# Kernel optimization log

Measured on AMD Instinct MI355X. Metric: run time of the kernel, lower is better.

Reference implementation:

```python
import jax, jax.numpy as jnp
import numpy as np

# ---- static config (matches init_kwargs) ----
B, S, D = 2, 4096, 1024          # batch, seq_len, dim_input
L, ST = 512, 64                  # segment_len, state_len
H = 8                            # num_heads
DK0, DV0, DK1, DV1 = 64, 64, 64, 64  # per-head key/value dims for 2 memory levels
DH = 4096                        # dim_hidden (MLP)
T = 2 * ST + L                   # tokens per segment block: [state, segment, state]


def setup_inputs() -> dict:
    key = jax.random.key(0)
    ks = jax.random.split(key, 18)
    f32 = jnp.float32
    def w(k, shape, fan_in):
        return (jax.random.normal(k, shape, dtype=f32) / np.float32(np.sqrt(fan_in)))
    return {
        "x": jax.random.normal(ks[0], (B, S, D), dtype=f32),
        "state_init": 0.02 * jax.random.normal(ks[1], (ST, D), dtype=f32),
        # level-0 projections: dim_input -> per-head (key/value)
        "Wq0": w(ks[2], (D, H, DK0), D),
        "Wk0": w(ks[3], (D, H, DK0), D),
        "Wv0": w(ks[4], (D, H, DV0), D),
        # level-1 projections: level-0 value dim -> per-head (key/value)
        "Wq1": w(ks[5], (H, DV0, DK1), DV0),
        "Wk1": w(ks[6], (H, DV0, DK1), DV0),
        "Wv1": w(ks[7], (H, DV0, DV1), DV0),
        # output projection back to dim_input
        "Wo": w(ks[8], (H, DV1, D), H * DV1),
        "bo": jnp.zeros((D,), f32),
        "g_attn": jnp.ones((D,), f32),
        "b_attn": jnp.zeros((D,), f32),
        "W1": w(ks[9], (D, DH), D),
        "b1": jnp.zeros((DH,), f32),
        "W2": w(ks[10], (DH, D), DH),
        "b2": jnp.zeros((D,), f32),
        "g_mlp": jnp.ones((D,), f32),
        "b_mlp": jnp.zeros((D,), f32),
    }


def _layernorm(x, g, b, eps=1e-5):
    mu = jnp.mean(x, axis=-1, keepdims=True)
    var = jnp.mean(jnp.square(x - mu), axis=-1, keepdims=True)
    return (x - mu) * jax.lax.rsqrt(var + eps) * g + b


def _rope(x, pos):
    # x: (B, H, T, dk); rotary embedding with base 10000
    dk = x.shape[-1]
    inv_freq = jnp.power(jnp.float32(10000.0), -jnp.arange(0, dk, 2, dtype=jnp.float32) / dk)
    ang = pos[:, None] * inv_freq[None, :]              # (T, dk/2)
    cos, sin = jnp.cos(ang), jnp.sin(ang)
    x1, x2 = x[..., 0::2], x[..., 1::2]
    r1 = x1 * cos - x2 * sin
    r2 = x1 * sin + x2 * cos
    return jnp.stack([r1, r2], axis=-1).reshape(x.shape)


def _attend(q, k, v, mask):
    # q,k: (B,H,T,dk); v: (B,H,T,dv); causal mask (T,T)
    scale = jnp.float32(1.0 / np.sqrt(q.shape[-1]))
    scores = jnp.einsum('bhqc,bhkc->bhqk', q, k) * scale
    scores = jnp.where(mask, scores, jnp.float32(-1e30))
    p = jax.nn.softmax(scores, axis=-1)
    return jnp.einsum('bhqk,bhkv->bhqv', p, v)


def _remmtas(x, state_init, Wq0, Wk0, Wv0, Wq1, Wk1, Wv1, Wo, bo):
    b, s, d = x.shape
    n_seg = s // L
    xs = x.reshape(b, n_seg, L, d).transpose(1, 0, 2, 3)   # (n_seg, B, L, D)
    mask = jnp.tril(jnp.ones((T, T), dtype=bool))
    pos = jnp.arange(T, dtype=jnp.float32)
    state0 = jnp.broadcast_to(state_init, (b, ST, d))

    def step(state, seg):
        toks = jnp.concatenate([state, seg, state], axis=1)      # (B, T, D)
        # memory level 0
        q0 = _rope(jnp.einsum('btd,dhk->bhtk', toks, Wq0), pos)
        k0 = _rope(jnp.einsum('btd,dhk->bhtk', toks, Wk0), pos)
        v0 = jnp.einsum('btd,dhv->bhtv', toks, Wv0)
        o0 = _attend(q0, k0, v0, mask)                           # (B,H,T,DV0)
        # memory level 1 (consumes level-0 values, per-head)
        q1 = _rope(jnp.einsum('bhtv,hvk->bhtk', o0, Wq1), pos)
        k1 = _rope(jnp.einsum('bhtv,hvk->bhtk', o0, Wk1), pos)
        v1 = jnp.einsum('bhtv,hvw->bhtw', o0, Wv1)
        o1 = _attend(q1, k1, v1, mask)                           # (B,H,T,DV1)
        out = jnp.einsum('bhtv,hvd->btd', o1, Wo) + bo           # (B,T,D)
        new_state = out[:, ST + L:]                              # trailing state tokens
        return new_state, out[:, ST:ST + L]                      # segment output

    _, outs = jax.lax.scan(step, state0, xs)                     # (n_seg, B, L, D)
    return outs.transpose(1, 0, 2, 3).reshape(b, s, d)


def reference(x, state_init, Wq0, Wk0, Wv0, Wq1, Wk1, Wv1, Wo, bo,
              g_attn, b_attn, W1, b1, W2, b2, g_mlp, b_mlp):
    a = _remmtas(x, state_init, Wq0, Wk0, Wv0, Wq1, Wk1, Wv1, Wo, bo)
    h = _layernorm(a + x, g_attn, b_attn)
    m = jax.nn.gelu(h @ W1 + b1, approximate=False) @ W2 + b2
    # note: second residual adds the ORIGINAL x, per the source code
    return _layernorm(m + x, g_mlp, b_mlp)
```

## Files before the change

kernel.cpp:

```cpp
#include <hip/hip_runtime.h>
#include <hip/hip_bf16.h>

typedef __hip_bfloat16 bf16;
typedef short bf16x8 __attribute__((ext_vector_type(8)));
typedef float f32x4 __attribute__((ext_vector_type(4)));

#define CB 2
#define CS 4096
#define CD 1024
#define CL 512
#define CST 64
#define CH 8
#define CT 640
#define CDH 4096
#define NSEG 8
#define MCH 2048
#define LP 80

__device__ __forceinline__ float tof(float x) { return x; }
__device__ __forceinline__ float tof(bf16 x) { return __bfloat162float(x); }
__device__ __forceinline__ void storev(float* p, float v) { *p = v; }
__device__ __forceinline__ void storev(bf16* p, float v) { *p = __float2bfloat16(v); }

__device__ __forceinline__ float ldin(const void* p, size_t i, int f32w) {
    if (f32w) return ((const float*)p)[i];
    return __bfloat162float(((const bf16*)p)[i]);
}

__global__ void sniff_kernel(const void* x, int* flag) {
    if (threadIdx.x == 0 && blockIdx.x == 0) {
        const bf16* hb = (const bf16*)x;
        int plaus = 0;
        for (int i = 0; i < 256; ++i) {
            float v = __bfloat162float(hb[2 * i]);
            float a = fabsf(v);
            if (v == 0.f || (a > 1e-4f && a < 100.f)) ++plaus;
        }
        flag[0] = (plaus < 128) ? 1 : 0;
    }
}

__global__ __launch_bounds__(256) void transpose_kernel(
    const void* __restrict__ in, bf16* __restrict__ out, int R, int C,
    const int* __restrict__ flag)
{
    const int f32w = flag[0];
    __shared__ short t[64][72];
    int tid = threadIdx.x;
    int c0 = blockIdx.x * 64, r0 = blockIdx.y * 64;
    int cc = tid & 63, rr = tid >> 6;
#pragma unroll
    for (int i = 0; i < 16; ++i) {
        bf16 v = __float2bfloat16(ldin(in, (size_t)(r0 + rr + i * 4) * C + c0 + cc, f32w));
        t[rr + i * 4][cc] = *(short*)&v;
    }
    __syncthreads();
#pragma unroll
    for (int i = 0; i < 16; ++i)
        ((short*)out)[(size_t)(c0 + rr + i * 4) * R + r0 + cc] = t[cc][rr + i * 4];
}

__global__ __launch_bounds__(256) void transposeH_kernel(
    const void* __restrict__ Wq1, const void* __restrict__ Wk1, const void* __restrict__ Wv1,
    bf16* __restrict__ oq, bf16* __restrict__ ok, bf16* __restrict__ ov,
    const int* __restrict__ flag)
{
    const int f32w = flag[0];
    int which = blockIdx.x >> 3, hh = blockIdx.x & 7;
    const void* in = (which == 0) ? Wq1 : (which == 1) ? Wk1 : Wv1;
    bf16* out = (which == 0) ? oq : (which == 1) ? ok : ov;
    __shared__ short t[64][72];
    int tid = threadIdx.x;
    int cc = tid & 63, rr = tid >> 6;
    size_t base = (size_t)hh * 4096;
#pragma unroll
    for (int i = 0; i < 16; ++i) {
        bf16 v = __float2bfloat16(ldin(in, base + (size_t)(rr + i * 4) * 64 + cc, f32w));
        t[rr + i * 4][cc] = *(short*)&v;
    }
    __syncthreads();
#pragma unroll
    for (int i = 0; i < 16; ++i)
        ((short*)out)[base + (size_t)(rr + i * 4) * 64 + cc] = t[cc][rr + i * 4];
}

template <typename TC, int ACT, int OUTM, int KSPLIT>
__global__ __launch_bounds__(256) void mfma_lds(
    const bf16* __restrict__ A,
    const bf16* __restrict__ Bt0, const bf16* __restrict__ Bt1, const bf16* __restrict__ Bt2,
    TC* __restrict__ C0, TC* __restrict__ C1, TC* __restrict__ C2,
    const void* __restrict__ bias, int M, int N, int K, int seg,
    const int* __restrict__ flag)
{
    const int f32w = flag[0];
    const bf16* Bt = (blockIdx.z == 0) ? Bt0 : (blockIdx.z == 1 ? Bt1 : Bt2);
    TC* C = (blockIdx.z == 0) ? C0 : (blockIdx.z == 1 ? C1 : C2);
    const int kz = (KSPLIT > 1) ? (int)blockIdx.z : 0;
    const int kbeg = (KSPLIT > 1) ? kz * (K / KSPLIT) : 0;
    const int kend = (KSPLIT > 1) ? kbeg + K / KSPLIT : K;

    __shared__ __align__(16) short As[128 * 64];
    __shared__ __align__(16) short Bs[128 * 64];

    const int tid = threadIdx.x;
    const int lane = tid & 63;
    const int w = tid >> 6;
    const int wm = w >> 1, wn = w & 1;
    const int bm = blockIdx.x * 128, bn = blockIdx.y * 128;

    f32x4 acc[4][4];
#pragma unroll
    for (int i = 0; i < 4; ++i)
#pragma unroll
        for (int j = 0; j < 4; ++j) acc[i][j] = (f32x4){0.f, 0.f, 0.f, 0.f};

    bf16x8 rA[4], rB[4];
#pragma unroll
    for (int i = 0; i < 4; ++i) {
        int c = i * 256 + tid;
        int row = c >> 3, kc = c & 7;
        rA[i] = *(const bf16x8*)(A + (size_t)(bm + row) * K + kbeg + kc * 8);
        rB[i] = *(const bf16x8*)(Bt + (size_t)(bn + row) * K + kbeg + kc * 8);
    }

    for (int k0 = kbeg; k0 < kend; k0 += 64) {
        __syncthreads();
#pragma unroll
        for (int i = 0; i < 4; ++i) {
            *(bf16x8*)&As[(size_t)(i * 256 + tid) * 8] = rA[i];
            *(bf16x8*)&Bs[(size_t)(i * 256 + tid) * 8] = rB[i];
        }
        if (k0 + 64 < kend) {
            int kn = k0 + 64;
#pragma unroll
            for (int i = 0; i < 4; ++i) {
                int c = i * 256 + tid;
                int row = c >> 3, kc = c & 7;
                rA[i] = *(const bf16x8*)(A + (size_t)(bm + row) * K + kn + kc * 8);
                rB[i] = *(const bf16x8*)(Bt + (size_t)(bn + row) * K + kn + kc * 8);
            }
        }
        __syncthreads();

#pragma unroll
        for (int kh = 0; kh < 2; ++kh) {
            bf16x8 av[4], bv[4];
#pragma unroll
            for (int mi = 0; mi < 4; ++mi) {
                int r = wm * 64 + mi * 16 + (lane & 15);
                int cl = kh * 4 + (lane >> 4);
                av[mi] = *(const bf16x8*)&As[r * 64 + cl * 8];
            }
#pragma unroll
            for (int nj = 0; nj < 4; ++nj) {
                int r = wn * 64 + nj * 16 + (lane & 15);
                int cl = kh * 4 + (lane >> 4);
                bv[nj] = *(const bf16x8*)&Bs[r * 64 + cl * 8];
            }
#pragma unroll
            for (int mi = 0; mi < 4; ++mi)
#pragma unroll
                for (int nj = 0; nj < 4; ++nj)
                    acc[mi][nj] = __builtin_amdgcn_mfma_f32_16x16x32_bf16(
                        av[mi], bv[nj], acc[mi][nj], 0, 0, 0);
        }
    }

#pragma unroll
    for (int mi = 0; mi < 4; ++mi) {
#pragma unroll
        for (int nj = 0; nj < 4; ++nj) {
            int c = bn + wn * 64 + nj * 16 + (lane & 15);
            float bia = (bias && kz == 0) ? ldin(bias, c, f32w) : 0.f;
#pragma unroll
            for (int r = 0; r < 4; ++r) {
                int row = bm + wm * 64 + mi * 16 + (lane >> 4) * 4 + r;
                float v = acc[mi][nj][r] + bia;
                if (ACT == 1) v = 0.5f * v * (1.0f + erff(v * 0.70710678118654752f));
                if (KSPLIT > 1) {
                    atomicAdd((float*)C + (size_t)row * N + c, v);
                } else if (OUTM == 0) {
                    storev(C + (size_t)row * N + c, v);
                } else {
                    int bb2 = row / CT, t = row % CT;
                    if (t >= CST) {
                        if (t < CST + CL)
                            storev(C0 + ((size_t)bb2 * CS + (size_t)seg * CL + (t - CST)) * CD + c, v);
                        else
                            storev(C1 + ((size_t)bb2 * CST + (t - CST - CL)) * CD + c, v);
                    }
                }
            }
        }
    }
}

__global__ __launch_bounds__(256) void ropeV_kernel(
    bf16* __restrict__ q, bf16* __restrict__ k,
    const bf16* __restrict__ v, bf16* __restrict__ vt)
{
    int t0 = blockIdx.x * 64, hh = blockIdx.y, b = blockIdx.z;
    int tid = threadIdx.x;
    __shared__ short lt[64][72];
    int c = tid & 63;
    int r0 = tid >> 6;
    int ip = c >> 1;
    float inv = powf(10000.f, -(float)(2 * ip) / 64.f);
#pragma unroll
    for (int i = 0; i < 16; ++i) {
        int r = r0 + i * 4;
        int t = t0 + r;
        size_t idx = ((size_t)b * CT + t) * 512 + hh * 64 + c;
        float qv = tof(q[idx]);
        float kv = tof(k[idx]);
        float ang = (float)t * inv;
        float sn, cs;
        sincosf(ang, &sn, &cs);
        float qp = __shfl_xor(qv, 1);
        float kp = __shfl_xor(kv, 1);
        float rq, rk;
        if (c & 1) { rq = qp * sn + qv * cs; rk = kp * sn + kv * cs; }
        else       { rq = qv * cs - qp * sn; rk = kv * cs - kp * sn; }
        q[idx] = __float2bfloat16(rq);
        k[idx] = __float2bfloat16(rk);
        lt[r][c] = ((const short*)v)[idx];
    }
    __syncthreads();
#pragma unroll
    for (int i = 0; i < 16; ++i) {
        int c2 = r0 + i * 4;
        int r2 = c;
        ((short*)vt)[((size_t)(b * CH + hh) * 64 + c2) * CT + t0 + r2] = lt[r2][c2];
    }
}

template <int FUSE>
__global__ __launch_bounds__(256) void attn_mfma(
    const bf16* __restrict__ q, const bf16* __restrict__ k, const bf16* __restrict__ vt,
    bf16* __restrict__ o,
    int qsb, int qsh, int qst,
    int ksb, int ksh, int kst,
    int ob, int oh, int ot,
    const bf16* __restrict__ Wq1t, const bf16* __restrict__ Wk1t, const bf16* __restrict__ Wv1t,
    bf16* __restrict__ q1o, bf16* __restrict__ k1o, bf16* __restrict__ v1to)
{
    const int tid = threadIdx.x;
    const int lane = tid & 63;
    const int wrow = tid >> 6;
    const int hh = blockIdx.y, b = blockIdx.z;
    const int qbase = ((int)gridDim.x - 1 - (int)blockIdx.x) * 64;

    __shared__ __align__(16) short Qs[64 * LP];
    __shared__ __align__(16) short Ks[64 * LP];
    __shared__ __align__(16) short Vs[64 * LP];
    __shared__ __align__(16) short Ps[64 * LP];

    const size_t qb0 = (size_t)b * qsb + (size_t)hh * qsh;
    const size_t kb0 = (size_t)b * ksb + (size_t)hh * ksh;
    const size_t vtb = (size_t)(b * CH + hh) * 64 * CT;

    int srow[2], skc[2], soff[2];
#pragma unroll
    for (int i = 0; i < 2; ++i) {
        int c = i * 256 + tid;
        srow[i] = c >> 3;
        skc[i] = c & 7;
        soff[i] = srow[i] * LP + skc[i] * 8;
    }

    bf16x8 rQ[2], rK[2], rV[2];
#pragma unroll
    for (int i = 0; i < 2; ++i) {
        rQ[i] = *(const bf16x8*)(q + qb0 + (size_t)(qbase + srow[i]) * qst + skc[i] * 8);
        rK[i] = *(const bf16x8*)(k + kb0 + (size_t)srow[i] * kst + skc[i] * 8);
        rV[i] = *(const bf16x8*)(vt + vtb + (size_t)srow[i] * CT + skc[i] * 8);
    }

    float mrow[4], lrow[4];
    f32x4 oacc[4];
#pragma unroll
    for (int r = 0; r < 4; ++r) { mrow[r] = -1e30f; lrow[r] = 0.f; }
#pragma unroll
    for (int nd = 0; nd < 4; ++nd) oacc[nd] = (f32x4){0.f, 0.f, 0.f, 0.f};

    const int ntiles = qbase / 64 + 1;
    for (int ti = 0; ti < ntiles; ++ti) {
        __syncthreads();
        if (ti == 0) {
#pragma unroll
            for (int i = 0; i < 2; ++i) *(bf16x8*)&Qs[soff[i]] = rQ[i];
        }
#pragma unroll
        for (int i = 0; i < 2; ++i) {
            *(bf16x8*)&Ks[soff[i]] = rK[i];
            *(bf16x8*)&Vs[soff[i]] = rV[i];
        }
        if (ti + 1 < ntiles) {
            int j1 = (ti + 1) * 64;
#pragma unroll
            for (int i = 0; i < 2; ++i) {
                rK[i] = *(const bf16x8*)(k + kb0 + (size_t)(j1 + srow[i]) * kst + skc[i] * 8);
                rV[i] = *(const bf16x8*)(vt + vtb + (size_t)srow[i] * CT + j1 + skc[i] * 8);
            }
        }
        __syncthreads();

        f32x4 sacc[4];
#pragma unroll
        for (int nj = 0; nj < 4; ++nj) sacc[nj] = (f32x4){0.f, 0.f, 0.f, 0.f};
#pragma unroll
        for (int kh = 0; kh < 2; ++kh) {
            int cl = kh * 4 + (lane >> 4);
            bf16x8 av = *(const bf16x8*)&Qs[(wrow * 16 + (lane & 15)) * LP + cl * 8];
#pragma unroll
            for (int nj = 0; nj < 4; ++nj) {
                bf16x8 bv = *(const bf16x8*)&Ks[(nj * 16 + (lane & 15)) * LP + cl * 8];
                sacc[nj] = __builtin_amdgcn_mfma_f32_16x16x32_bf16(av, bv, sacc[nj], 0, 0, 0);
            }
        }

        const bool diag = (ti == ntiles - 1);
        float pm[4] = {-1e30f, -1e30f, -1e30f, -1e30f};
#pragma unroll
        for (int nj = 0; nj < 4; ++nj) {
            int col_l = nj * 16 + (lane & 15);
#pragma unroll
            for (int r = 0; r < 4; ++r) {
                int row_l = wrow * 16 + ((lane >> 4) << 2) + r;
                float s = (diag && col_l > row_l) ? -1e30f : sacc[nj][r] * 0.125f;
                sacc[nj][r] = s;
                pm[r] = fmaxf(pm[r], s);
            }
        }
#pragma unroll
        for (int msk = 1; msk < 16; msk <<= 1)
#pragma unroll
            for (int r = 0; r < 4; ++r) pm[r] = fmaxf(pm[r], __shfl_xor(pm[r], msk));

        float corr[4], rs[4] = {0.f, 0.f, 0.f, 0.f};
#pragma unroll
        for (int r = 0; r < 4; ++r) {
            float mn = fmaxf(mrow[r], pm[r]);
            corr[r] = __expf(mrow[r] - mn);
            mrow[r] = mn;
        }
#pragma unroll
        for (int nj = 0; nj < 4; ++nj)
#pragma unroll
            for (int r = 0; r < 4; ++r) {
                float p = __expf(sacc[nj][r] - mrow[r]);
                sacc[nj][r] = p;
                rs[r] += p;
            }
#pragma unroll
        for (int msk = 1; msk < 16; msk <<= 1)
#pragma unroll
            for (int r = 0; r < 4; ++r) rs[r] += __shfl_xor(rs[r], msk);
#pragma unroll
        for (int r = 0; r < 4; ++r) lrow[r] = lrow[r] * corr[r] + rs[r];
#pragma unroll
        for (int nd = 0; nd < 4; ++nd)
#pragma unroll
            for (int r = 0; r < 4; ++r) oacc[nd][r] *= corr[r];

#pragma unroll
        for (int nj = 0; nj < 4; ++nj)
#pragma unroll
            for (int r = 0; r < 4; ++r) {
                bf16 pb = __float2bfloat16(sacc[nj][r]);
                Ps[(wrow * 16 + ((lane >> 4) << 2) + r) * LP + nj * 16 + (lane & 15)] =
                    *(short*)&pb;
            }

#pragma unroll
        for (int kh = 0; kh < 2; ++kh) {
            int cl = kh * 4 + (lane >> 4);
            bf16x8 pa = *(const bf16x8*)&Ps[(wrow * 16 + (lane & 15)) * LP + cl * 8];
#pragma unroll
            for (int nd = 0; nd < 4; ++nd) {
                bf16x8 bv = *(const bf16x8*)&Vs[(nd * 16 + (lane & 15)) * LP + cl * 8];
                oacc[nd] = __builtin_amdgcn_mfma_f32_16x16x32_bf16(pa, bv, oacc[nd], 0, 0, 0);
            }
        }
    }

    if (FUSE == 0) {
#pragma unroll
        for (int nd = 0; nd < 4; ++nd) {
#pragma unroll
            for (int r = 0; r < 4; ++r) {
                int row_g = qbase + wrow * 16 + ((lane >> 4) << 2) + r;
                int col = nd * 16 + (lane & 15);
                storev(&o[(size_t)b * ob + (size_t)hh * oh + (size_t)row_g * ot + col],
                       oacc[nd][r] / lrow[r]);
            }
        }
    } else {
#pragma unroll
        for (int nd = 0; nd < 4; ++nd)
#pragma unroll
            for (int r = 0; r < 4; ++r) {
                int row_l = wrow * 16 + ((lane >> 4) << 2) + r;
                bf16 ob16 = __float2bfloat16(oacc[nd][r] / lrow[r]);
                Qs[row_l * LP + nd * 16 + (lane & 15)] = *(short*)&ob16;
            }
        __syncthreads();

        const size_t whb = (size_t)hh * 4096;
        f32x4 qa[4], ka[4], va[4];
#pragma unroll
        for (int nj = 0; nj < 4; ++nj) {
            qa[nj] = (f32x4){0.f, 0.f, 0.f, 0.f};
            ka[nj] = (f32x4){0.f, 0.f, 0.f, 0.f};
            va[nj] = (f32x4){0.f, 0.f, 0.f, 0.f};
        }
#pragma unroll
        for (int kh = 0; kh < 2; ++kh) {
            int cl = kh * 4 + (lane >> 4);
            bf16x8 av = *(const bf16x8*)&Qs[(wrow * 16 + (lane & 15)) * LP + cl * 8];
#pragma unroll
            for (int nj = 0; nj < 4; ++nj) {
                int rowb = nj * 16 + (lane & 15);
                bf16x8 bq = *(const bf16x8*)(Wq1t + whb + (size_t)rowb * 64 + cl * 8);
                bf16x8 bk = *(const bf16x8*)(Wk1t + whb + (size_t)rowb * 64 + cl * 8);
                bf16x8 bw = *(const bf16x8*)(Wv1t + whb + (size_t)rowb * 64 + cl * 8);
                qa[nj] = __builtin_amdgcn_mfma_f32_16x16x32_bf16(av, bq, qa[nj], 0, 0, 0);
                ka[nj] = __builtin_amdgcn_mfma_f32_16x16x32_bf16(av, bk, ka[nj], 0, 0, 0);
                va[nj] = __builtin_amdgcn_mfma_f32_16x16x32_bf16(av, bw, va[nj], 0, 0, 0);
            }
        }
        const size_t bh = (size_t)(b * CH + hh);
#pragma unroll
        for (int nj = 0; nj < 4; ++nj) {
            int col = nj * 16 + (lane & 15);
            int ip = col >> 1;
            float inv = powf(10000.f, -(float)(2 * ip) / 64.f);
#pragma unroll
            for (int r = 0; r < 4; ++r) {
                int row_l = wrow * 16 + ((lane >> 4) << 2) + r;
                int t = qbase + row_l;
                float ang = (float)t * inv;
                float sn, cs;
                sincosf(ang, &sn, &cs);
                float aq = qa[nj][r], ak = ka[nj][r];
                float pq = __shfl_xor(aq, 1);
                float pk = __shfl_xor(ak, 1);
                float rq, rk;
                if (col & 1) { rq = pq * sn + aq * cs; rk = pk * sn + ak * cs; }
                else         { rq = aq * cs - pq * sn; rk = ak * cs - pk * sn; }
                size_t roff = (bh * CT + t) * 64 + col;
                q1o[roff] = __float2bfloat16(rq);
                k1o[roff] = __float2bfloat16(rk);
                v1to[(bh * 64 + col) * CT + t] = __float2bfloat16(va[nj][r]);
            }
        }
    }
}

__global__ __launch_bounds__(256) void build_toks_kernel(
    const void* __restrict__ x, const float* __restrict__ state, bf16* __restrict__ toks,
    int seg, const int* __restrict__ flag)
{
    const int f32w = flag[0];
    int idx = blockIdx.x * 256 + threadIdx.x;
    int d = idx & (CD - 1);
    int t = (idx >> 10) % CT;
    int b = idx / (CT * CD);
    float v;
    if (t < CST) v = state[(b * CST + t) * CD + d];
    else if (t < CST + CL) v = ldin(x, ((size_t)b * CS + seg * CL + (t - CST)) * CD + d, f32w);
    else v = state[(b * CST + (t - CST - CL)) * CD + d];
    toks[idx] = __float2bfloat16(v);
}

__global__ __launch_bounds__(256) void init_state_kernel(
    const void* __restrict__ s0, float* __restrict__ state, const int* __restrict__ flag)
{
    const int f32w = flag[0];
    int idx = blockIdx.x * 256 + threadIdx.x;
    state[idx] = ldin(s0, idx % (CST * CD), f32w);
}

__global__ __launch_bounds__(256) void ln_kernel(
    const float* __restrict__ ra, const void* __restrict__ x,
    const void* __restrict__ g, const void* __restrict__ bb,
    void* __restrict__ outp, int out_ext, const int* __restrict__ flag)
{
    const int f32w = flag[0];
    int row = blockIdx.x;
    int tid = threadIdx.x;
    __shared__ float buf[CD];
    __shared__ float red[4];

    float s = 0.f;
    for (int c = tid; c < CD; c += 256) {
        float v = ra[(size_t)row * CD + c] + ldin(x, (size_t)row * CD + c, f32w);
        buf[c] = v;
        s += v;
    }
#pragma unroll
    for (int off = 32; off; off >>= 1) s += __shfl_xor(s, off);
    if ((tid & 63) == 0) red[tid >> 6] = s;
    __syncthreads();
    float mu = (red[0] + red[1] + red[2] + red[3]) * (1.f / CD);
    __syncthreads();

    float vs = 0.f;
    for (int c = tid; c < CD; c += 256) {
        float d0 = buf[c] - mu;
        vs += d0 * d0;
    }
#pragma unroll
    for (int off = 32; off; off >>= 1) vs += __shfl_xor(vs, off);
    if ((tid & 63) == 0) red[tid >> 6] = vs;
    __syncthreads();
    float var = (red[0] + red[1] + red[2] + red[3]) * (1.f / CD);
    float rs = rsqrtf(var + 1e-5f);

    for (int c = tid; c < CD; c += 256) {
        float y = (buf[c] - mu) * rs * ldin(g, c, f32w) + ldin(bb, c, f32w);
        size_t idx = (size_t)row * CD + c;
        if (!out_ext) {
            ((bf16*)outp)[idx] = __float2bfloat16(y);
        } else if (f32w) {
            ((float*)outp)[idx] = y;
        } else {
            ((bf16*)outp)[idx] = __float2bfloat16(y);
        }
    }
}

extern "C" void kernel_launch(void* const* d_in, const int* in_sizes, int n_in,
                              void* d_out, int out_size, void* d_ws, size_t ws_size,
                              hipStream_t stream)
{
    const void* x      = d_in[0];
    const void* s0     = d_in[1];
    const void* Wq0    = d_in[2];
    const void* Wk0    = d_in[3];
    const void* Wv0    = d_in[4];
    const void* Wq1    = d_in[5];
    const void* Wk1    = d_in[6];
    const void* Wv1    = d_in[7];
    const void* Wo     = d_in[8];
    const void* bo     = d_in[9];
    const void* g_attn = d_in[10];
    const void* b_attn = d_in[11];
    const void* W1     = d_in[12];
    const void* b1     = d_in[13];
    const void* W2     = d_in[14];
    const void* b2     = d_in[15];
    const void* g_mlp  = d_in[16];
    const void* b_mlp  = d_in[17];

    int* flag = (int*)d_ws;
    float* f = (float*)((char*)d_ws + 16);
    float* toks_slot = f; f += (size_t)CB * CT * CD;
    float* q0_slot = f;  f += (size_t)CB * CH * CT * 64;
    float* k0_slot = f;  f += (size_t)CB * CH * CT * 64;
    float* v0_slot = f;  f += (size_t)CB * CH * CT * 64;
    float* o0_slot = f;  f += (size_t)CB * CH * CT * 64;
    float* q1_slot = f;  f += (size_t)CB * CH * CT * 64;
    float* k1_slot = f;  f += (size_t)CB * CH * CT * 64;
    float* v1_slot = f;  f += (size_t)CB * CH * CT * 64;
    float* o1t_slot = f; f += (size_t)CB * CT * (CH * 64);
    float* seg_slot = f; f += (size_t)CB * CT * CD;
    float* state = f;   f += (size_t)CB * CST * CD;
    float* a = f;       f += (size_t)CB * CS * CD;
    bf16* h = (bf16*)f;
    bf16* tail = h + (size_t)CB * CS * CD;

    bf16* toks = (bf16*)toks_slot;
    bf16* q0b = (bf16*)q0_slot;
    bf16* k0b = (bf16*)k0_slot;
    bf16* v0b = (bf16*)v0_slot;
    bf16* v0t = (bf16*)o0_slot;
    bf16* q1b = (bf16*)q1_slot;
    bf16* k1b = (bf16*)k1_slot;
    bf16* v1t = (bf16*)v1_slot;
    bf16* o1t = (bf16*)o1t_slot;
    bf16* WtQ = h;
    bf16* WtK = WtQ + (size_t)512 * 1024;
    bf16* WtV = WtK + (size_t)512 * 1024;
    bf16* WtO = WtV + (size_t)512 * 1024;
    bf16* WtQ1 = WtO + (size_t)1024 * 512;
    bf16* WtK1 = WtQ1 + (size_t)8 * 4096;
    bf16* WtV1 = WtK1 + (size_t)8 * 4096;
    bf16* g1  = (bf16*)toks_slot;
    bf16* Wt1 = g1 + (size_t)MCH * CDH;
    bf16* Wt2 = tail;

    sniff_kernel<<<1, 64, 0, stream>>>(x, flag);
    init_state_kernel<<<(CB * CST * CD) / 256, 256, 0, stream>>>(s0, state, flag);

    transpose_kernel<<<dim3(8, 16), 256, 0, stream>>>(Wq0, WtQ, CD, 512, flag);
    transpose_kernel<<<dim3(8, 16), 256, 0, stream>>>(Wk0, WtK, CD, 512, flag);
    transpose_kernel<<<dim3(8, 16), 256, 0, stream>>>(Wv0, WtV, CD, 512, flag);
    transpose_kernel<<<dim3(16, 8), 256, 0, stream>>>(Wo, WtO, 512, CD, flag);
    transposeH_kernel<<<24, 256, 0, stream>>>(Wq1, Wk1, Wv1, WtQ1, WtK1, WtV1, flag);

    for (int seg = 0; seg < NSEG; ++seg) {
        build_toks_kernel<<<(CB * CT * CD) / 256, 256, 0, stream>>>(x, state, toks, seg, flag);
        mfma_lds<bf16, 0, 0, 1><<<dim3(10, 4, 3), 256, 0, stream>>>(
            toks, WtQ, WtK, WtV, q0b, k0b, v0b, nullptr, CB * CT, 512, CD, 0, flag);
        ropeV_kernel<<<dim3(CT / 64, CH, CB), 256, 0, stream>>>(q0b, k0b, v0b, v0t);
        attn_mfma<1><<<dim3(CT / 64, CH, CB), 256, 0, stream>>>(
            q0b, k0b, v0t, nullptr,
            CT * 512, 64, 512,
            CT * 512, 64, 512,
            0, 0, 0,
            WtQ1, WtK1, WtV1, q1b, k1b, v1t);
        attn_mfma<0><<<dim3(CT / 64, CH, CB), 256, 0, stream>>>(
            q1b, k1b, v1t, o1t,
            CH * CT * 64, CT * 64, 64,
            CH * CT * 64, CT * 64, 64,
            CT * 512, 64, 512,
            nullptr, nullptr, nullptr, nullptr, nullptr, nullptr);
        mfma_lds<float, 0, 1, 1><<<dim3(10, 8, 1), 256, 0, stream>>>(
            o1t, WtO, WtO, WtO, a, state, a, bo, CB * CT, CD, 512, seg, flag);
    }

    ln_kernel<<<CB * CS, 256, 0, stream>>>(a, x, g_attn, b_attn, h, 0, flag);

    transpose_kernel<<<dim3(CDH / 64, CD / 64), 256, 0, stream>>>(W1, Wt1, CD, CDH, flag);
    transpose_kernel<<<dim3(CD / 64, CDH / 64), 256, 0, stream>>>(W2, Wt2, CDH, CD, flag);

    for (int c = 0; c < (CB * CS) / MCH; ++c) {
        mfma_lds<bf16, 1, 0, 1><<<dim3(MCH / 128, CDH / 128, 1), 256, 0, stream>>>(
            h + (size_t)c * MCH * CD, Wt1, Wt1, Wt1, g1, g1, g1, b1, MCH, CDH, CD, 0, flag);
        mfma_lds<float, 0, 0, 1><<<dim3(MCH / 128, CD / 128, 1), 256, 0, stream>>>(
            g1, Wt2, Wt2, Wt2,
            a + (size_t)c * MCH * CD, a + (size_t)c * MCH * CD, a + (size_t)c * MCH * CD,
            b2, MCH, CD, CDH, 0, flag);
    }
    ln_kernel<<<CB * CS, 256, 0, stream>>>(a, x, g_mlp, b_mlp, d_out, 1, flag);
}
```

Before: 1.333 ms.

## Fuse token build and RoPE into QKV GEMM; chunk MLP over hidden dim

Replaces the per-segment build_toks, QKV GEMM and ropeV kernels with one mfma_qkv kernel. It gathers x/state rows directly as the A operand, and applies RoPE and the V transpose in the epilogue. The MLP is now chunked along the hidden dimension (four 1024-wide slices over all 8192 rows) instead of along rows, and the second GEMM accumulates into the output by read-modify-write. This removes kernel launches and intermediate round-trips, and gives larger grids. The cost is extra reads of the accumulator in later MLP chunks and per-element sincos/powf in the GEMM epilogue.

New measurement: 1.571 ms. 17.8% more time.

```diff
diff --git a/kernel.cpp b/kernel.cpp
--- a/kernel.cpp
+++ b/kernel.cpp
@@ -14,7 +14,6 @@
 #define CT 640
 #define CDH 4096
 #define NSEG 8
-#define MCH 2048
 #define LP 80
 
 __device__ __forceinline__ float tof(float x) { return x; }
@@ -84,20 +83,18 @@
         ((short*)out)[base + (size_t)(rr + i * 4) * 64 + cc] = t[cc][rr + i * 4];
 }
 
-template <typename TC, int ACT, int OUTM, int KSPLIT>
+template <typename TC, int ACT, int OUTM, int ACCUM>
 __global__ __launch_bounds__(256) void mfma_lds(
     const bf16* __restrict__ A,
     const bf16* __restrict__ Bt0, const bf16* __restrict__ Bt1, const bf16* __restrict__ Bt2,
     TC* __restrict__ C0, TC* __restrict__ C1, TC* __restrict__ C2,
-    const void* __restrict__ bias, int M, int N, int K, int seg,
+    const void* __restrict__ bias, int boff,
+    int M, int N, int K, int lda, int ldb, int seg,
     const int* __restrict__ flag)
 {
     const int f32w = flag[0];
     const bf16* Bt = (blockIdx.z == 0) ? Bt0 : (blockIdx.z == 1 ? Bt1 : Bt2);
     TC* C = (blockIdx.z == 0) ? C0 : (blockIdx.z == 1 ? C1 : C2);
-    const int kz = (KSPLIT > 1) ? (int)blockIdx.z : 0;
-    const int kbeg = (KSPLIT > 1) ? kz * (K / KSPLIT) : 0;
-    const int kend = (KSPLIT > 1) ? kbeg + K / KSPLIT : K;
 
     __shared__ __align__(16) short As[128 * 64];
     __shared__ __align__(16) short Bs[128 * 64];
@@ -119,25 +116,25 @@
     for (int i = 0; i < 4; ++i) {
         int c = i * 256 + tid;
         int row = c >> 3, kc = c & 7;
-        rA[i] = *(const bf16x8*)(A + (size_t)(bm + row) * K + kbeg + kc * 8);
-        rB[i] = *(const bf16x8*)(Bt + (size_t)(bn + row) * K + kbeg + kc * 8);
-    }
-
-    for (int k0 = kbeg; k0 < kend; k0 += 64) {
+        rA[i] = *(const bf16x8*)(A + (size_t)(bm + row) * lda + kc * 8);
+        rB[i] = *(const bf16x8*)(Bt + (size_t)(bn + row) * ldb + kc * 8);
+    }
+
+    for (int k0 = 0; k0 < K; k0 += 64) {
         __syncthreads();
 #pragma unroll
         for (int i = 0; i < 4; ++i) {
             *(bf16x8*)&As[(size_t)(i * 256 + tid) * 8] = rA[i];
             *(bf16x8*)&Bs[(size_t)(i * 256 + tid) * 8] = rB[i];
         }
-        if (k0 + 64 < kend) {
+        if (k0 + 64 < K) {
             int kn = k0 + 64;
 #pragma unroll
             for (int i = 0; i < 4; ++i) {
                 int c = i * 256 + tid;
                 int row = c >> 3, kc = c & 7;
-                rA[i] = *(const bf16x8*)(A + (size_t)(bm + row) * K + kn + kc * 8);
-                rB[i] = *(const bf16x8*)(Bt + (size_t)(bn + row) * K + kn + kc * 8);
+                rA[i] = *(const bf16x8*)(A + (size_t)(bm + row) * lda + kn + kc * 8);
+                rB[i] = *(const bf16x8*)(Bt + (size_t)(bn + row) * ldb + kn + kc * 8);
             }
         }
         __syncthreads();
@@ -171,15 +168,14 @@
 #pragma unroll
         for (int nj = 0; nj < 4; ++nj) {
             int c = bn + wn * 64 + nj * 16 + (lane & 15);
-            float bia = (bias && kz == 0) ? ldin(bias, c, f32w) : 0.f;
+            float bia = bias ? ldin(bias, boff + c, f32w) : 0.f;
 #pragma unroll
             for (int r = 0; r < 4; ++r) {
                 int row = bm + wm * 64 + mi * 16 + (lane >> 4) * 4 + r;
                 float v = acc[mi][nj][r] + bia;
                 if (ACT == 1) v = 0.5f * v * (1.0f + erff(v * 0.70710678118654752f));
-                if (KSPLIT > 1) {
-                    atomicAdd((float*)C + (size_t)row * N + c, v);
-                } else if (OUTM == 0) {
+                if (OUTM == 0) {
+                    if (ACCUM) v += tof(C[(size_t)row * N + c]);
                     storev(C + (size_t)row * N + c, v);
                 } else {
                     int bb2 = row / CT, t = row % CT;
@@ -195,42 +191,139 @@
     }
 }
 
-__global__ __launch_bounds__(256) void ropeV_kernel(
-    bf16* __restrict__ q, bf16* __restrict__ k,
-    const bf16* __restrict__ v, bf16* __restrict__ vt)
+__global__ __launch_bounds__(256) void mfma_qkv(
+    const void* __restrict__ x, const float* __restrict__ state,
+    const bf16* __restrict__ WtQ, const bf16* __restrict__ WtK, const bf16* __restrict__ WtV,
+    bf16* __restrict__ q0, bf16* __restrict__ k0, bf16* __restrict__ v0t,
+    int seg, const int* __restrict__ flag)
 {
-    int t0 = blockIdx.x * 64, hh = blockIdx.y, b = blockIdx.z;
-    int tid = threadIdx.x;
-    __shared__ short lt[64][72];
-    int c = tid & 63;
-    int r0 = tid >> 6;
-    int ip = c >> 1;
-    float inv = powf(10000.f, -(float)(2 * ip) / 64.f);
-#pragma unroll
-    for (int i = 0; i < 16; ++i) {
-        int r = r0 + i * 4;
-        int t = t0 + r;
-        size_t idx = ((size_t)b * CT + t) * 512 + hh * 64 + c;
-        float qv = tof(q[idx]);
-        float kv = tof(k[idx]);
-        float ang = (float)t * inv;
-        float sn, cs;
-        sincosf(ang, &sn, &cs);
-        float qp = __shfl_xor(qv, 1);
-        float kp = __shfl_xor(kv, 1);
-        float rq, rk;
-        if (c & 1) { rq = qp * sn + qv * cs; rk = kp * sn + kv * cs; }
-        else       { rq = qv * cs - qp * sn; rk = kv * cs - kp * sn; }
-        q[idx] = __float2bfloat16(rq);
-        k[idx] = __float2bfloat16(rk);
-        lt[r][c] = ((const short*)v)[idx];
-    }
-    __syncthreads();
-#pragma unroll
-    for (int i = 0; i < 16; ++i) {
-        int c2 = r0 + i * 4;
-        int r2 = c;
-        ((short*)vt)[((size_t)(b * CH + hh) * 64 + c2) * CT + t0 + r2] = lt[r2][c2];
+    const int f32w = flag[0];
+    const bf16* Bt = (blockIdx.z == 0) ? WtQ : (blockIdx.z == 1 ? WtK : WtV);
+
+    __shared__ __align__(16) short As[128 * 64];
+    __shared__ __align__(16) short Bs[128 * 64];
+
+    const int tid = threadIdx.x;
+    const int lane = tid & 63;
+    const int w = tid >> 6;
+    const int wm = w >> 1, wn = w & 1;
+    const int bm = blockIdx.x * 128, bn = blockIdx.y * 128;
+
+    auto loadA = [&](int mrow, int d0) -> bf16x8 {
+        int b = mrow / CT, t = mrow % CT;
+        bf16x8 r;
+        if (t >= CST && t < CST + CL) {
+            size_t idx = ((size_t)b * CS + (size_t)seg * CL + (t - CST)) * CD + d0;
+            if (!f32w) {
+                r = *(const bf16x8*)((const bf16*)x + idx);
+            } else {
+                const float* p = (const float*)x + idx;
+                float4 f0 = *(const float4*)p, f1 = *(const float4*)(p + 4);
+                float vv[8] = {f0.x, f0.y, f0.z, f0.w, f1.x, f1.y, f1.z, f1.w};
+#pragma unroll
+                for (int j = 0; j < 8; ++j) { bf16 v = __float2bfloat16(vv[j]); r[j] = *(short*)&v; }
+            }
+        } else {
+            int ts = (t < CST) ? t : (t - CST - CL);
+            const float* p = state + ((size_t)b * CST + ts) * CD + d0;
+            float4 f0 = *(const float4*)p, f1 = *(const float4*)(p + 4);
+            float vv[8] = {f0.x, f0.y, f0.z, f0.w, f1.x, f1.y, f1.z, f1.w};
+#pragma unroll
+            for (int j = 0; j < 8; ++j) { bf16 v = __float2bfloat16(vv[j]); r[j] = *(short*)&v; }
+        }
+        return r;
+    };
+
+    f32x4 acc[4][4];
+#pragma unroll
+    for (int i = 0; i < 4; ++i)
+#pragma unroll
+        for (int j = 0; j < 4; ++j) acc[i][j] = (f32x4){0.f, 0.f, 0.f, 0.f};
+
+    bf16x8 rA[4], rB[4];
+#pragma unroll
+    for (int i = 0; i < 4; ++i) {
+        int c = i * 256 + tid;
+        int row = c >> 3, kc = c & 7;
+        rA[i] = loadA(bm + row, kc * 8);
+        rB[i] = *(const bf16x8*)(Bt + (size_t)(bn + row) * CD + kc * 8);
+    }
+
+    for (int kk0 = 0; kk0 < CD; kk0 += 64) {
+        __syncthreads();
+#pragma unroll
+        for (int i = 0; i < 4; ++i) {
+            *(bf16x8*)&As[(size_t)(i * 256 + tid) * 8] = rA[i];
+            *(bf16x8*)&Bs[(size_t)(i * 256 + tid) * 8] = rB[i];
+        }
+        if (kk0 + 64 < CD) {
+            int kn = kk0 + 64;
+#pragma unroll
+            for (int i = 0; i < 4; ++i) {
+                int c = i * 256 + tid;
+                int row = c >> 3, kc = c & 7;
+                rA[i] = loadA(bm + row, kn + kc * 8);
+                rB[i] = *(const bf16x8*)(Bt + (size_t)(bn + row) * CD + kn + kc * 8);
+            }
+        }
+        __syncthreads();
+
+#pragma unroll
+        for (int kh = 0; kh < 2; ++kh) {
+            bf16x8 av[4], bv[4];
+#pragma unroll
+            for (int mi = 0; mi < 4; ++mi) {
+                int r = wm * 64 + mi * 16 + (lane & 15);
+                int cl = kh * 4 + (lane >> 4);
+                av[mi] = *(const bf16x8*)&As[r * 64 + cl * 8];
+            }
+#pragma unroll
+            for (int nj = 0; nj < 4; ++nj) {
+                int r = wn * 64 + nj * 16 + (lane & 15);
+                int cl = kh * 4 + (lane >> 4);
+                bv[nj] = *(const bf16x8*)&Bs[r * 64 + cl * 8];
+            }
+#pragma unroll
+            for (int mi = 0; mi < 4; ++mi)
+#pragma unroll
+                for (int nj = 0; nj < 4; ++nj)
+                    acc[mi][nj] = __builtin_amdgcn_mfma_f32_16x16x32_bf16(
+                        av[mi], bv[nj], acc[mi][nj], 0, 0, 0);
+        }
+    }
+
+    const int isV = (blockIdx.z == 2);
+#pragma unroll
+    for (int mi = 0; mi < 4; ++mi) {
+#pragma unroll
+        for (int nj = 0; nj < 4; ++nj) {
+            int col = bn + wn * 64 + nj * 16 + (lane & 15);
+            if (!isV) {
+                int ip = (col & 63) >> 1;
+                float inv = powf(10000.f, -(float)(2 * ip) / 64.f);
+                bf16* dst = (blockIdx.z == 0) ? q0 : k0;
+#pragma unroll
+                for (int r = 0; r < 4; ++r) {
+                    int row = bm + wm * 64 + mi * 16 + (lane >> 4) * 4 + r;
+                    int t = row % CT;
+                    float av = acc[mi][nj][r];
+                    float pv = __shfl_xor(av, 1);
+                    float ang = (float)t * inv;
+                    float sn, cs;
+                    sincosf(ang, &sn, &cs);
+                    float rv = (col & 1) ? (pv * sn + av * cs) : (av * cs - pv * sn);
+                    dst[(size_t)row * 512 + col] = __float2bfloat16(rv);
+                }
+            } else {
+#pragma unroll
+                for (int r = 0; r < 4; ++r) {
+                    int row = bm + wm * 64 + mi * 16 + (lane >> 4) * 4 + r;
+                    int b = row / CT, t = row % CT;
+                    v0t[(((size_t)(b * CH) + (col >> 6)) * 64 + (col & 63)) * CT + t] =
+                        __float2bfloat16(acc[mi][nj][r]);
+                }
+            }
+        }
     }
 }
 
@@ -455,22 +548,6 @@
             }
         }
     }
-}
-
-__global__ __launch_bounds__(256) void build_toks_kernel(
-    const void* __restrict__ x, const float* __restrict__ state, bf16* __restrict__ toks,
-    int seg, const int* __restrict__ flag)
-{
-    const int f32w = flag[0];
-    int idx = blockIdx.x * 256 + threadIdx.x;
-    int d = idx & (CD - 1);
-    int t = (idx >> 10) % CT;
-    int b = idx / (CT * CD);
-    float v;
-    if (t < CST) v = state[(b * CST + t) * CD + d];
-    else if (t < CST + CL) v = ldin(x, ((size_t)b * CS + seg * CL + (t - CST)) * CD + d, f32w);
-    else v = state[(b * CST + (t - CST - CL)) * CD + d];
-    toks[idx] = __float2bfloat16(v);
 }
 
 __global__ __launch_bounds__(256) void init_state_kernel(
@@ -570,10 +647,8 @@
     bf16* h = (bf16*)f;
     bf16* tail = h + (size_t)CB * CS * CD;
 
-    bf16* toks = (bf16*)toks_slot;
     bf16* q0b = (bf16*)q0_slot;
     bf16* k0b = (bf16*)k0_slot;
-    bf16* v0b = (bf16*)v0_slot;
     bf16* v0t = (bf16*)o0_slot;
     bf16* q1b = (bf16*)q1_slot;
     bf16* k1b = (bf16*)k1_slot;
@@ -587,7 +662,7 @@
     bf16* WtK1 = WtQ1 + (size_t)8 * 4096;
     bf16* WtV1 = WtK1 + (size_t)8 * 4096;
     bf16* g1  = (bf16*)toks_slot;
-    bf16* Wt1 = g1 + (size_t)MCH * CDH;
+    bf16* Wt1 = g1 + (size_t)CS * CB * CD;
     bf16* Wt2 = tail;
 
     sniff_kernel<<<1, 64, 0, stream>>>(x, flag);
@@ -600,10 +675,8 @@
     transposeH_kernel<<<24, 256, 0, stream>>>(Wq1, Wk1, Wv1, WtQ1, WtK1, WtV1, flag);
 
     for (int seg = 0; seg < NSEG; ++seg) {
-        build_toks_kernel<<<(CB * CT * CD) / 256, 256, 0, stream>>>(x, state, toks, seg, flag);
-        mfma_lds<bf16, 0, 0, 1><<<dim3(10, 4, 3), 256, 0, stream>>>(
-            toks, WtQ, WtK, WtV, q0b, k0b, v0b, nullptr, CB * CT, 512, CD, 0, flag);
-        ropeV_kernel<<<dim3(CT / 64, CH, CB), 256, 0, stream>>>(q0b, k0b, v0b, v0t);
+        mfma_qkv<<<dim3(10, 4, 3), 256, 0, stream>>>(
+            x, state, WtQ, WtK, WtV, q0b, k0b, v0t, seg, flag);
         attn_mfma<1><<<dim3(CT / 64, CH, CB), 256, 0, stream>>>(
             q0b, k0b, v0t, nullptr,
             CT * 512, 64, 512,
@@ -616,8 +689,9 @@
             CH * CT * 64, CT * 64, 64,
             CT * 512, 64, 512,
             nullptr, nullptr, nullptr, nullptr, nullptr, nullptr);
-        mfma_lds<float, 0, 1, 1><<<dim3(10, 8, 1), 256, 0, stream>>>(
-            o1t, WtO, WtO, WtO, a, state, a, bo, CB * CT, CD, 512, seg, flag);
+        mfma_lds<float, 0, 1, 0><<<dim3(10, 8, 1), 256, 0, stream>>>(
+            o1t, WtO, WtO, WtO, a, state, a, bo, 0,
+            CB * CT, CD, 512, 512, 512, seg, flag);
     }
 
     ln_kernel<<<CB * CS, 256, 0, stream>>>(a, x, g_attn, b_attn, h, 0, flag);
@@ -625,13 +699,18 @@
     transpose_kernel<<<dim3(CDH / 64, CD / 64), 256, 0, stream>>>(W1, Wt1, CD, CDH, flag);
     transpose_kernel<<<dim3(CD / 64, CDH / 64), 256, 0, stream>>>(W2, Wt2, CDH, CD, flag);
 
-    for (int c = 0; c < (CB * CS) / MCH; ++c) {
-        mfma_lds<bf16, 1, 0, 1><<<dim3(MCH / 128, CDH / 128, 1), 256, 0, stream>>>(
-            h + (size_t)c * MCH * CD, Wt1, Wt1, Wt1, g1, g1, g1, b1, MCH, CDH, CD, 0, flag);
-        mfma_lds<float, 0, 0, 1><<<dim3(MCH / 128, CD / 128, 1), 256, 0, stream>>>(
-            g1, Wt2, Wt2, Wt2,
-            a + (size_t)c * MCH * CD, a + (size_t)c * MCH * CD, a + (size_t)c * MCH * CD,
-            b2, MCH, CD, CDH, 0, flag);
+    for (int c = 0; c < 4; ++c) {
+        mfma_lds<bf16, 1, 0, 0><<<dim3(64, 8, 1), 256, 0, stream>>>(
+            h, Wt1 + (size_t)c * 1024 * CD, Wt1, Wt1, g1, g1, g1,
+            b1, c * 1024, CB * CS, 1024, CD, CD, CD, 0, flag);
+        if (c == 0)
+            mfma_lds<float, 0, 0, 0><<<dim3(64, 8, 1), 256, 0, stream>>>(
+                g1, Wt2 + (size_t)c * 1024, Wt2, Wt2, a, a, a,
+                b2, 0, CB * CS, CD, 1024, 1024, CDH, 0, flag);
+        else
+            mfma_lds<float, 0, 0, 1><<<dim3(64, 8, 1), 256, 0, stream>>>(
+                g1, Wt2 + (size_t)c * 1024, Wt2, Wt2, a, a, a,
+                nullptr, 0, CB * CS, CD, 1024, 1024, CDH, 0, flag);
     }
     ln_kernel<<<CB * CS, 256, 0, stream>>>(a, x, g_mlp, b_mlp, d_out, 1, flag);
 }
```
